# Kernel tuning notes

Hardware: AMD Instinct MI355X
Metric: run time of the kernel (lower is better)

## Reference

```python
import jax, jax.numpy as jnp
import numpy as np

SMOOTH = 1e-06
LAMBDA_FOCAL = 1.0
LAMBDA_DICE = 1.0
LAMBDA_BOUNDARY = 0.5
LAMBDA_CONTRASTIVE = 0.1
ALPHA = 0.25
GAMMA = 2.0
NUM_IDS = 32  # instance ids in [0, NUM_IDS); 0 = background


def _sobel_grad(x):
    """Kornia-style normalized sobel spatial gradient with replicate padding.
    x: [B,1,H,W] -> (gx, gy) each [B,1,H,W]."""
    kx = jnp.array([[-1., 0., 1.], [-2., 0., 2.], [-1., 0., 1.]], x.dtype) / 8.0  # abs-sum normalized
    ky = kx.T
    k = jnp.stack([kx, ky])[:, None]  # [2,1,3,3]
    xp = jnp.pad(x, ((0, 0), (0, 0), (1, 1), (1, 1)), mode='edge')
    out = jax.lax.conv_general_dilated(xp, k, (1, 1), 'VALID',
                                       dimension_numbers=('NCHW', 'OIHW', 'NCHW'))
    return out[:, 0:1], out[:, 1:2]


def _forward(predictions, targets, instance_masks):
    p = jnp.clip(jax.nn.sigmoid(predictions), SMOOTH, 1.0 - SMOOTH)  # [B,H,W]
    t = jnp.clip(targets, 0.0, 1.0)

    # ---- focal loss ----
    bce = -(t * jnp.log(p) + (1.0 - t) * jnp.log1p(-p))
    pt = jnp.where(t == 1.0, p, 1.0 - p)
    focal_w = (1.0 - pt) ** GAMMA
    alpha_w = jnp.where(t == 1.0, ALPHA, 1.0 - ALPHA)
    focal = jnp.mean(alpha_w * focal_w * bce)

    # ---- dice loss ----
    inter = jnp.sum(p * t)
    dice = 1.0 - (2.0 * inter + SMOOTH) / (jnp.sum(p) + jnp.sum(t) + SMOOTH)

    # ---- boundary loss (sobel gradient magnitude + direction) ----
    p4, t4 = p[:, None], t[:, None]  # [B,1,H,W]
    tgx, tgy = _sobel_grad(t4)
    pgx, pgy = _sobel_grad(p4)
    tmag = jnp.sqrt(tgx ** 2 + tgy ** 2 + 1e-6)
    pmag = jnp.sqrt(pgx ** 2 + pgy ** 2 + 1e-6)
    bw = 1.0 + 5.0 * tmag
    loss_mag = jnp.mean((pmag * bw - tmag * bw) ** 2)
    mask = (tmag > 0.1).astype(p.dtype)
    cos = (tgx / tmag) * (pgx / pmag) + (tgy / tmag) * (pgy / pmag)
    msum = jnp.sum(mask)
    dir_loss = jnp.where(msum > 0, jnp.sum((1.0 - cos) * mask) / jnp.maximum(msum, 1.0), 0.0)
    boundary = loss_mag + dir_loss

    # ---- instance contrastive loss (segment-mean + pairwise exp distance) ----
    B = p.shape[0]
    ids = instance_masks.reshape(B, -1).astype(jnp.int32)
    flat_ids = (ids + jnp.arange(B, dtype=jnp.int32)[:, None] * NUM_IDS).reshape(-1)
    pf = p.reshape(-1)
    sums = jax.ops.segment_sum(pf, flat_ids, num_segments=B * NUM_IDS).reshape(B, NUM_IDS)
    cnts = jax.ops.segment_sum(jnp.ones_like(pf), flat_ids, num_segments=B * NUM_IDS).reshape(B, NUM_IDS)
    means = sums / jnp.maximum(cnts, 1.0)  # [B,K]
    ks = jnp.arange(NUM_IDS)
    valid = (cnts > 0) & (ks[None, :] > 0)  # exclude background id 0
    diff = jnp.abs(means[:, :, None] - means[:, None, :])  # [B,K,K]
    pair = (valid[:, :, None] & valid[:, None, :] & (ks[:, None] < ks[None, :])).astype(p.dtype)
    npairs = jnp.sum(pair, axis=(1, 2))
    csum = jnp.sum(jnp.exp(-diff) * pair, axis=(1, 2))
    contrastive = jnp.sum(jnp.where(npairs > 0, csum / jnp.maximum(npairs, 1.0), 0.0)) / B

    return (LAMBDA_FOCAL * focal + LAMBDA_DICE * dice
            + LAMBDA_BOUNDARY * boundary + LAMBDA_CONTRASTIVE * contrastive)


def setup_inputs() -> dict:
    key = jax.random.key(0)
    k1, k2, k3 = jax.random.split(key, 3)
    B, H, W = 16, 1024, 1024
    predictions = jax.random.normal(k1, (B, H, W), dtype=jnp.float32)
    targets = jnp.round(jax.random.uniform(k2, (B, H, W), dtype=jnp.float32))  # binary masks
    instance_masks = jax.random.randint(k3, (B, H, W), 0, NUM_IDS, dtype=jnp.int32)
    return {"predictions": predictions, "targets": targets, "instance_masks": instance_masks}


def reference(predictions, targets, instance_masks):
    return _forward(predictions, targets, instance_masks)
```

## Files before the change

kernel.cpp:

```cpp
#include <hip/hip_runtime.h>
#include <math.h>

#define HH 1024
#define WW 1024
#define BB 16
#define RR 8
#define NID 32
#define NPX (1ull * BB * HH * WW)
#define CBIT 41
#define SSCALE 262144.0f
#define INV_SSCALE 3.814697265625e-06f


__device__ __forceinline__ float fast_rcp(float x) {
  float r; asm("v_rcp_f32 %0, %1" : "=v"(r) : "v"(x)); return r;
}
__device__ __forceinline__ float fast_rsq(float x) {
  float r; asm("v_rsq_f32 %0, %1" : "=v"(r) : "v"(x)); return r;
}
__device__ __forceinline__ float sigc(float x) {
  return fast_rcp(1.f + __expf(-x));
}

__global__ __launch_bounds__(256, 3) void seg_main(
    const float* __restrict__ pred, const float* __restrict__ targ,
    const int* __restrict__ ids, float* __restrict__ acc,
    unsigned long long* __restrict__ seg_pack) {
  __shared__ unsigned long long s_pack[NID];
  __shared__ float red[4][8];
  __shared__ float2 ttab[256];

  const int tid = threadIdx.x;
  const int b  = blockIdx.x >> 7;
  const int rg = blockIdx.x & 127;
  const int h0 = rg * RR;
  const int w0 = tid * 4;
  const int wl = (w0 == 0) ? 0 : w0 - 1;
  const int wr = (w0 == WW - 4) ? WW - 1 : w0 + 4;

  if (tid < NID) s_pack[tid] = 0ull;
  {
    float tgx = fmaf((float)(tid & 15), 0.125f, -0.5f);
    float tgy = fmaf((float)(tid >> 4), 0.125f, -0.5f);
    float m2t = tgx * tgx + tgy * tgy + 1e-6f;
    float rst = fast_rsq(m2t);
    ttab[tid] = make_float2(m2t * rst, rst);
  }
  __syncthreads();

  const size_t base = (size_t)b * HH * WW;
  const float*  pb  = pred + base;
  const float*  tb  = targ + base;
  const int4*   ib4 = (const int4*)(ids + base);

  float facc = 0.f, iacc = 0.f, pacc = 0.f, macc = 0.f, dacc = 0.f;
  int   tcnt = 0, kcnt = 0;

  float Pa0, Pa1, Pa2, Pa3, Pa4, Pa5, Ha1, Ha2, Ha3, Ha4;
  float Pb0, Pb1, Pb2, Pb3, Pb4, Pb5, Hb1, Hb2, Hb3, Hb4;
  float Pc0, Pc1, Pc2, Pc3, Pc4, Pc5, Hc1, Hc2, Hc3, Hc4;
  unsigned int Na, Nb, Nc, HDa, HDb, HDc;
  float4 nx, nt;
  float nxl, nxr, ntl, ntr;
  int4 IDa, IDb;

#define LOADRAW(h)                                                     \
  do { int hh = (h); hh = hh < 0 ? 0 : (hh > HH - 1 ? HH - 1 : hh);    \
    const float* pr  = pb + hh * WW;                                   \
    const float* trw = tb + hh * WW;                                   \
    nx  = *(const float4*)(pr + w0);                                   \
    nxl = pr[wl];  nxr = pr[wr];                                       \
    nt  = *(const float4*)(trw + w0);                                  \
    ntl = trw[wl]; ntr = trw[wr];                                      \
  } while (0)

#define SIG(P, H, N, HD)                                               \
  do {                                                                 \
    P##0 = sigc(nxl);  P##1 = sigc(nx.x); P##2 = sigc(nx.y);           \
    P##3 = sigc(nx.z); P##4 = sigc(nx.w); P##5 = sigc(nxr);            \
    H##1 = P##2 - P##0; H##2 = P##3 - P##1;                            \
    H##3 = P##4 - P##2; H##4 = P##5 - P##3;                            \
    N = (ntl  >= 0.5f ? 0x1u      : 0u)                                \
      | (nt.x >= 0.5f ? 0x10u     : 0u)                                \
      | (nt.y >= 0.5f ? 0x100u    : 0u)                                \
      | (nt.z >= 0.5f ? 0x1000u   : 0u)                                \
      | (nt.w >= 0.5f ? 0x10000u  : 0u)                                \
      | (ntr  >= 0.5f ? 0x100000u : 0u);                               \
    HD = ((N >> 4) + 0x011110u) - (N << 4);                            \
  } while (0)

#define PIX(PB, HA, HB, HC, NB_, GX, GY, c0, c1, c2, idj)              \
  do {                                                                 \
    float p = PB##c1;                                                  \
    const int one = (int)((NB_ >> (4 * (c1))) & 1u);                   \
    float pt = one ? p : 1.f - p;                                      \
    float om = 1.f - pt;                                               \
    facc += (one ? 0.25f : 0.75f) * om * om * (-__logf(pt));           \
    iacc += one ? p : 0.f;                                             \
    pacc += p;                                                         \
    unsigned int gxb = (GX >> (4 * (c1))) & 15u;                       \
    unsigned int gyb = (GY >> (4 * (c1))) & 15u;                       \
    unsigned int tix = gxb | (gyb << 4);                               \
    float2 tt = ttab[tix];               \
    float tmag = tt.x, rst = tt.y;                                     \
    float pgx = (HA##c1 + HC##c1 + 2.f * HB##c1) * 0.125f;             \
    float pgy = (vd##c0 + vd##c2 + 2.f * vd##c1) * 0.125f;             \
    float m2p = pgx * pgx + pgy * pgy + 1e-6f;                         \
    float rsp = fast_rsq(m2p);                                         \
    float pmag = m2p * rsp;                                            \
    float bwv = fmaf(tmag, 5.f, 1.f);                                  \
    float d = (pmag - tmag) * bwv;                                     \
    macc += d * d;                                                     \
    if (tix != 0x44u) {                                                \
      float tgx = fmaf((float)gxb, 0.125f, -0.5f);                     \
      float tgy = fmaf((float)gyb, 0.125f, -0.5f);                     \
      dacc += 1.f - (tgx * pgx + tgy * pgy) * (rst * rsp);             \
      kcnt += 1;                                                       \
    }                                                                  \
    unsigned int q = __float2uint_rn(p * SSCALE);                      \
    atomicAdd(&s_pack[idj], (1ull << CBIT) | (unsigned long long)q);   \
  } while (0)

#define BODY(PA, PB, PC, HA, HB, HC, NA_, NB_, NC_, HDA_, HDB_, HDC_,  \
             IDU, IDN, r)                                              \
  do {                                                                 \
    SIG(PC, HC, NC_, HDC_);                                            \
    if ((r) < RR - 1) {                                                \
      LOADRAW(h0 + (r) + 2);                                           \
      IDN = ib4[(h0 + (r) + 1) * (WW / 4) + tid];                      \
    }                                                                  \
    unsigned int GX = HDA_ + (HDB_ << 1) + HDC_;           \
    unsigned int VD = (NC_ + 0x111111u) - NA_;             \
    unsigned int GY = (VD << 4) + (VD << 1) + (VD >> 4);   \
    tcnt += __popc(NB_ & 0x011110u);                                   \
    float vd0 = PC##0 - PA##0, vd1 = PC##1 - PA##1;                    \
    float vd2 = PC##2 - PA##2, vd3 = PC##3 - PA##3;                    \
    float vd4 = PC##4 - PA##4, vd5 = PC##5 - PA##5;                    \
    PIX(PB, HA, HB, HC, NB_, GX, GY, 0, 1, 2, IDU.x);                  \
    PIX(PB, HA, HB, HC, NB_, GX, GY, 1, 2, 3, IDU.y);                  \
    PIX(PB, HA, HB, HC, NB_, GX, GY, 2, 3, 4, IDU.z);                  \
    PIX(PB, HA, HB, HC, NB_, GX, GY, 3, 4, 5, IDU.w);                  \
    __builtin_amdgcn_sched_barrier(0);                                 \
  } while (0)

  LOADRAW(h0 - 1); SIG(Pa, Ha, Na, HDa);
  LOADRAW(h0);     SIG(Pb, Hb, Nb, HDb);
  LOADRAW(h0 + 1);
  IDa = ib4[h0 * (WW / 4) + tid];
  __builtin_amdgcn_sched_barrier(0);

  BODY(Pa, Pb, Pc, Ha, Hb, Hc, Na, Nb, Nc, HDa, HDb, HDc, IDa, IDb, 0);
  BODY(Pb, Pc, Pa, Hb, Hc, Ha, Nb, Nc, Na, HDb, HDc, HDa, IDb, IDa, 1);
  BODY(Pc, Pa, Pb, Hc, Ha, Hb, Nc, Na, Nb, HDc, HDa, HDb, IDa, IDb, 2);
  BODY(Pa, Pb, Pc, Ha, Hb, Hc, Na, Nb, Nc, HDa, HDb, HDc, IDb, IDa, 3);
  BODY(Pb, Pc, Pa, Hb, Hc, Ha, Nb, Nc, Na, HDb, HDc, HDa, IDa, IDb, 4);
  BODY(Pc, Pa, Pb, Hc, Ha, Hb, Nc, Na, Nb, HDc, HDa, HDb, IDb, IDa, 5);
  BODY(Pa, Pb, Pc, Ha, Hb, Hc, Na, Nb, Nc, HDa, HDb, HDc, IDa, IDb, 6);
  BODY(Pb, Pc, Pa, Hb, Hc, Ha, Nb, Nc, Na, HDb, HDc, HDa, IDb, IDa, 7);

#undef LOADRAW
#undef SIG
#undef PIX
#undef BODY

  float tacc = (float)tcnt;
  float kacc = (float)kcnt;
#define WRED(x)                                                        \
  do { _Pragma("unroll")                                               \
    for (int off = 32; off > 0; off >>= 1) x += __shfl_down(x, off, 64); \
  } while (0)
  WRED(facc); WRED(iacc); WRED(pacc); WRED(tacc);
  WRED(macc); WRED(dacc); WRED(kacc);
#undef WRED
  int wave = tid >> 6, lane = tid & 63;
  if (lane == 0) {
    red[wave][0] = facc; red[wave][1] = iacc; red[wave][2] = pacc;
    red[wave][3] = tacc; red[wave][4] = macc; red[wave][5] = dacc;
    red[wave][6] = kacc;
  }
  __syncthreads();
  if (tid < 7) {
    atomicAdd(&acc[tid], red[0][tid] + red[1][tid] + red[2][tid] + red[3][tid]);
  }
  if (tid < NID) {
    atomicAdd(&seg_pack[b * NID + tid], s_pack[tid]);
  }
}

__global__ void seg_final(const float* __restrict__ acc,
                          const unsigned long long* __restrict__ seg_pack,
                          float* __restrict__ out) {
  __shared__ float contr[BB];
  int tid = threadIdx.x;
  int b   = tid >> 4;
  int l16 = tid & 15;
  if (b < BB) {
    float means[NID];
    bool  val[NID];
    #pragma unroll
    for (int k = 0; k < NID; ++k) {
      unsigned long long v = seg_pack[b * NID + k];
      float cnt = (float)(v >> CBIT);
      float sum = (float)(v & ((1ull << CBIT) - 1)) * INV_SSCALE;
      means[k] = sum / fmaxf(cnt, 1.f);
      val[k] = (cnt > 0.f) && (k > 0);
    }
    float csum = 0.f, np = 0.f;
    int cnt = 0;
    #pragma unroll
    for (int k = 0; k < NID; ++k) {
      #pragma unroll
      for (int l = k + 1; l < NID; ++l) {
        if ((cnt & 15) == l16) {
          if (val[k] && val[l]) {
            csum += __expf(-fabsf(means[k] - means[l]));
            np += 1.f;
          }
        }
        ++cnt;
      }
    }
    #pragma unroll
    for (int off = 1; off < 16; off <<= 1) {
      csum += __shfl_xor(csum, off, 16);
      np   += __shfl_xor(np,   off, 16);
    }
    if (l16 == 0) contr[b] = (np > 0.f) ? csum / fmaxf(np, 1.f) : 0.f;
  }
  __syncthreads();
  if (tid == 0) {
    float c = 0.f;
    for (int b2 = 0; b2 < BB; ++b2) c += contr[b2];
    c /= (float)BB;
    float N = (float)NPX;
    float focal = acc[0] / N;
    float dice  = 1.f - (2.f * acc[1] + 1e-6f) / (acc[2] + acc[3] + 1e-6f);
    float dir   = (acc[6] > 0.f) ? acc[5] / fmaxf(acc[6], 1.f) : 0.f;
    float boundary = acc[4] / N + dir;
    out[0] = focal + dice + 0.5f * boundary + 0.1f * c;
  }
}

extern "C" void kernel_launch(void* const* d_in, const int* in_sizes, int n_in,
                              void* d_out, int out_size, void* d_ws, size_t ws_size,
                              hipStream_t stream) {
  const float* pred = (const float*)d_in[0];
  const float* targ = (const float*)d_in[1];
  const int*   ids  = (const int*)d_in[2];
  float* acc = (float*)d_ws;
  unsigned long long* seg_pack = (unsigned long long*)((char*)d_ws + 64);

  hipMemsetAsync(d_ws, 0, 64 + BB * NID * sizeof(unsigned long long), stream);

  int blocks = BB * (HH / RR);
  seg_main<<<blocks, 256, 0, stream>>>(pred, targ, ids, acc, seg_pack);
  seg_final<<<1, 256, 0, stream>>>(acc, seg_pack, (float*)d_out);
}
```

Before: 68.49 us.

## Process eight pixels per thread with 128-thread blocks and byte-packed ids

Each thread now covers eight consecutive columns instead of four, so blocks shrink to 128 threads. The halo loads and sigmoid evaluations on the left and right edges are shared across more pixels, and instance ids are packed into a 64-bit register of bytes. The aim is to cut redundant halo work and per-thread overhead. In exchange, register pressure rises, launch bounds drop to minimum one block, and each block has fewer waves, which may reduce occupancy and latency hiding.

```diff
diff --git a/kernel.cpp b/kernel.cpp
--- a/kernel.cpp
+++ b/kernel.cpp
@@ -11,6 +11,7 @@
 #define SSCALE 262144.0f
 #define INV_SSCALE 3.814697265625e-06f
 
+typedef unsigned long long u64;
 
 __device__ __forceinline__ float fast_rcp(float x) {
   float r; asm("v_rcp_f32 %0, %1" : "=v"(r) : "v"(x)); return r;
@@ -22,29 +23,33 @@
   return fast_rcp(1.f + __expf(-x));
 }
 
-__global__ __launch_bounds__(256, 3) void seg_main(
+__global__ __launch_bounds__(128, 1) void seg_main(
     const float* __restrict__ pred, const float* __restrict__ targ,
     const int* __restrict__ ids, float* __restrict__ acc,
     unsigned long long* __restrict__ seg_pack) {
   __shared__ unsigned long long s_pack[NID];
-  __shared__ float red[4][8];
+  __shared__ float red[2][8];
   __shared__ float2 ttab[256];
 
   const int tid = threadIdx.x;
   const int b  = blockIdx.x >> 7;
   const int rg = blockIdx.x & 127;
   const int h0 = rg * RR;
-  const int w0 = tid * 4;
+  const int w0 = tid * 8;
   const int wl = (w0 == 0) ? 0 : w0 - 1;
-  const int wr = (w0 == WW - 4) ? WW - 1 : w0 + 4;
+  const int wr = (w0 == WW - 8) ? WW - 1 : w0 + 8;
 
   if (tid < NID) s_pack[tid] = 0ull;
   {
-    float tgx = fmaf((float)(tid & 15), 0.125f, -0.5f);
-    float tgy = fmaf((float)(tid >> 4), 0.125f, -0.5f);
-    float m2t = tgx * tgx + tgy * tgy + 1e-6f;
-    float rst = fast_rsq(m2t);
-    ttab[tid] = make_float2(m2t * rst, rst);
+    #pragma unroll
+    for (int q = 0; q < 2; ++q) {
+      int e = tid + q * 128;
+      float tgx = fmaf((float)(e & 15), 0.125f, -0.5f);
+      float tgy = fmaf((float)(e >> 4), 0.125f, -0.5f);
+      float m2t = tgx * tgx + tgy * tgy + 1e-6f;
+      float rst = fast_rsq(m2t);
+      ttab[e] = make_float2(m2t * rst, rst);
+    }
   }
   __syncthreads();
 
@@ -56,55 +61,84 @@
   float facc = 0.f, iacc = 0.f, pacc = 0.f, macc = 0.f, dacc = 0.f;
   int   tcnt = 0, kcnt = 0;
 
-  float Pa0, Pa1, Pa2, Pa3, Pa4, Pa5, Ha1, Ha2, Ha3, Ha4;
-  float Pb0, Pb1, Pb2, Pb3, Pb4, Pb5, Hb1, Hb2, Hb3, Hb4;
-  float Pc0, Pc1, Pc2, Pc3, Pc4, Pc5, Hc1, Hc2, Hc3, Hc4;
-  unsigned int Na, Nb, Nc, HDa, HDb, HDc;
-  float4 nx, nt;
+  float Pa0, Pa1, Pa2, Pa3, Pa4, Pa5, Pa6, Pa7, Pa8, Pa9;
+  float Pb0, Pb1, Pb2, Pb3, Pb4, Pb5, Pb6, Pb7, Pb8, Pb9;
+  float Pc0, Pc1, Pc2, Pc3, Pc4, Pc5, Pc6, Pc7, Pc8, Pc9;
+  float Ha1, Ha2, Ha3, Ha4, Ha5, Ha6, Ha7, Ha8;
+  float Hb1, Hb2, Hb3, Hb4, Hb5, Hb6, Hb7, Hb8;
+  float Hc1, Hc2, Hc3, Hc4, Hc5, Hc6, Hc7, Hc8;
+  unsigned int NLa, NLb, NLc, NHa, NHb, NHc;
+  unsigned int DLa, DLb, DLc, DHa, DHb, DHc;
+  float4 nx0, nx1, nt0, nt1;
   float nxl, nxr, ntl, ntr;
-  int4 IDa, IDb;
+  u64 IDa, IDb;
 
 #define LOADRAW(h)                                                     \
   do { int hh = (h); hh = hh < 0 ? 0 : (hh > HH - 1 ? HH - 1 : hh);    \
     const float* pr  = pb + hh * WW;                                   \
     const float* trw = tb + hh * WW;                                   \
-    nx  = *(const float4*)(pr + w0);                                   \
+    nx0 = *(const float4*)(pr + w0);                                   \
+    nx1 = *(const float4*)(pr + w0 + 4);                               \
     nxl = pr[wl];  nxr = pr[wr];                                       \
-    nt  = *(const float4*)(trw + w0);                                  \
+    nt0 = *(const float4*)(trw + w0);                                  \
+    nt1 = *(const float4*)(trw + w0 + 4);                              \
     ntl = trw[wl]; ntr = trw[wr];                                      \
   } while (0)
 
-#define SIG(P, H, N, HD)                                               \
+#define LOADID(h, D)                                                   \
   do {                                                                 \
-    P##0 = sigc(nxl);  P##1 = sigc(nx.x); P##2 = sigc(nx.y);           \
-    P##3 = sigc(nx.z); P##4 = sigc(nx.w); P##5 = sigc(nxr);            \
-    H##1 = P##2 - P##0; H##2 = P##3 - P##1;                            \
-    H##3 = P##4 - P##2; H##4 = P##5 - P##3;                            \
-    N = (ntl  >= 0.5f ? 0x1u      : 0u)                                \
-      | (nt.x >= 0.5f ? 0x10u     : 0u)                                \
-      | (nt.y >= 0.5f ? 0x100u    : 0u)                                \
-      | (nt.z >= 0.5f ? 0x1000u   : 0u)                                \
-      | (nt.w >= 0.5f ? 0x10000u  : 0u)                                \
-      | (ntr  >= 0.5f ? 0x100000u : 0u);                               \
-    HD = ((N >> 4) + 0x011110u) - (N << 4);                            \
-  } while (0)
-
-#define PIX(PB, HA, HB, HC, NB_, GX, GY, c0, c1, c2, idj)              \
+    int4 qa = ib4[(h) * (WW / 4) + 2 * tid];                           \
+    int4 qb = ib4[(h) * (WW / 4) + 2 * tid + 1];                       \
+    unsigned int lo = (unsigned)qa.x | ((unsigned)qa.y << 8)           \
+                    | ((unsigned)qa.z << 16) | ((unsigned)qa.w << 24); \
+    unsigned int hi = (unsigned)qb.x | ((unsigned)qb.y << 8)           \
+                    | ((unsigned)qb.z << 16) | ((unsigned)qb.w << 24); \
+    D = (u64)lo | ((u64)hi << 32);                                     \
+  } while (0)
+
+#define SIG(C)                                                         \
   do {                                                                 \
-    float p = PB##c1;                                                  \
-    const int one = (int)((NB_ >> (4 * (c1))) & 1u);                   \
+    P##C##0 = sigc(nxl);   P##C##1 = sigc(nx0.x);                      \
+    P##C##2 = sigc(nx0.y); P##C##3 = sigc(nx0.z);                      \
+    P##C##4 = sigc(nx0.w); P##C##5 = sigc(nx1.x);                      \
+    P##C##6 = sigc(nx1.y); P##C##7 = sigc(nx1.z);                      \
+    P##C##8 = sigc(nx1.w); P##C##9 = sigc(nxr);                        \
+    H##C##1 = P##C##2 - P##C##0; H##C##2 = P##C##3 - P##C##1;          \
+    H##C##3 = P##C##4 - P##C##2; H##C##4 = P##C##5 - P##C##3;          \
+    H##C##5 = P##C##6 - P##C##4; H##C##6 = P##C##7 - P##C##5;          \
+    H##C##7 = P##C##8 - P##C##6; H##C##8 = P##C##9 - P##C##7;          \
+    NL##C = (ntl   >= 0.5f ? 0x1u      : 0u)                           \
+          | (nt0.x >= 0.5f ? 0x10u     : 0u)                           \
+          | (nt0.y >= 0.5f ? 0x100u    : 0u)                           \
+          | (nt0.z >= 0.5f ? 0x1000u   : 0u)                           \
+          | (nt0.w >= 0.5f ? 0x10000u  : 0u)                           \
+          | (nt1.x >= 0.5f ? 0x100000u : 0u);                          \
+    NH##C = (nt0.w >= 0.5f ? 0x1u      : 0u)                           \
+          | (nt1.x >= 0.5f ? 0x10u     : 0u)                           \
+          | (nt1.y >= 0.5f ? 0x100u    : 0u)                           \
+          | (nt1.z >= 0.5f ? 0x1000u   : 0u)                           \
+          | (nt1.w >= 0.5f ? 0x10000u  : 0u)                           \
+          | (ntr   >= 0.5f ? 0x100000u : 0u);                          \
+    DL##C = ((NL##C >> 4) + 0x011110u) - (NL##C << 4);                 \
+    DH##C = ((NH##C >> 4) + 0x011110u) - (NH##C << 4);                 \
+  } while (0)
+
+#define PIX(A, B, C, N_, GX_, GY_, nib, wa, wb, wc, k, IDU)            \
+  do {                                                                 \
+    float p = P##B##wb;                                                \
+    const int one = (int)((N_ >> (4 * (nib))) & 1u);                   \
     float pt = one ? p : 1.f - p;                                      \
     float om = 1.f - pt;                                               \
     facc += (one ? 0.25f : 0.75f) * om * om * (-__logf(pt));           \
     iacc += one ? p : 0.f;                                             \
     pacc += p;                                                         \
-    unsigned int gxb = (GX >> (4 * (c1))) & 15u;                       \
-    unsigned int gyb = (GY >> (4 * (c1))) & 15u;                       \
+    unsigned int gxb = (GX_ >> (4 * (nib))) & 15u;                     \
+    unsigned int gyb = (GY_ >> (4 * (nib))) & 15u;                     \
     unsigned int tix = gxb | (gyb << 4);                               \
     float2 tt = ttab[tix];               \
     float tmag = tt.x, rst = tt.y;                                     \
-    float pgx = (HA##c1 + HC##c1 + 2.f * HB##c1) * 0.125f;             \
-    float pgy = (vd##c0 + vd##c2 + 2.f * vd##c1) * 0.125f;             \
+    float pgx = (H##A##wb + H##C##wb + 2.f * H##B##wb) * 0.125f;       \
+    float pgy = (vd##wa + vd##wc + 2.f * vd##wb) * 0.125f;             \
     float m2p = pgx * pgx + pgy * pgy + 1e-6f;                         \
     float rsp = fast_rsq(m2p);                                         \
     float pmag = m2p * rsp;                                            \
@@ -117,48 +151,58 @@
       dacc += 1.f - (tgx * pgx + tgy * pgy) * (rst * rsp);             \
       kcnt += 1;                                                       \
     }                                                                  \
+    unsigned int idj = (unsigned int)(IDU >> (8 * (k))) & 31u;         \
     unsigned int q = __float2uint_rn(p * SSCALE);                      \
     atomicAdd(&s_pack[idj], (1ull << CBIT) | (unsigned long long)q);   \
   } while (0)
 
-#define BODY(PA, PB, PC, HA, HB, HC, NA_, NB_, NC_, HDA_, HDB_, HDC_,  \
-             IDU, IDN, r)                                              \
+#define BODY(A, B, C, IDU, IDN, r)                                     \
   do {                                                                 \
-    SIG(PC, HC, NC_, HDC_);                                            \
+    SIG(C);                                                            \
     if ((r) < RR - 1) {                                                \
       LOADRAW(h0 + (r) + 2);                                           \
-      IDN = ib4[(h0 + (r) + 1) * (WW / 4) + tid];                      \
+      LOADID(h0 + (r) + 1, IDN);                                       \
     }                                                                  \
-    unsigned int GX = HDA_ + (HDB_ << 1) + HDC_;           \
-    unsigned int VD = (NC_ + 0x111111u) - NA_;             \
-    unsigned int GY = (VD << 4) + (VD << 1) + (VD >> 4);   \
-    tcnt += __popc(NB_ & 0x011110u);                                   \
-    float vd0 = PC##0 - PA##0, vd1 = PC##1 - PA##1;                    \
-    float vd2 = PC##2 - PA##2, vd3 = PC##3 - PA##3;                    \
-    float vd4 = PC##4 - PA##4, vd5 = PC##5 - PA##5;                    \
-    PIX(PB, HA, HB, HC, NB_, GX, GY, 0, 1, 2, IDU.x);                  \
-    PIX(PB, HA, HB, HC, NB_, GX, GY, 1, 2, 3, IDU.y);                  \
-    PIX(PB, HA, HB, HC, NB_, GX, GY, 2, 3, 4, IDU.z);                  \
-    PIX(PB, HA, HB, HC, NB_, GX, GY, 3, 4, 5, IDU.w);                  \
+    unsigned int GXl = DL##A + (DL##B << 1) + DL##C;                   \
+    unsigned int VDl = (NL##C + 0x111111u) - NL##A;                    \
+    unsigned int GYl = (VDl << 4) + (VDl << 1) + (VDl >> 4);           \
+    unsigned int GXh = DH##A + (DH##B << 1) + DH##C;                   \
+    unsigned int VDh = (NH##C + 0x111111u) - NH##A;                    \
+    unsigned int GYh = (VDh << 4) + (VDh << 1) + (VDh >> 4);           \
+    tcnt += __popc(NL##B & 0x011110u) + __popc(NH##B & 0x011110u);     \
+    float vd0 = P##C##0 - P##A##0, vd1 = P##C##1 - P##A##1;            \
+    float vd2 = P##C##2 - P##A##2, vd3 = P##C##3 - P##A##3;            \
+    float vd4 = P##C##4 - P##A##4, vd5 = P##C##5 - P##A##5;            \
+    float vd6 = P##C##6 - P##A##6, vd7 = P##C##7 - P##A##7;            \
+    float vd8 = P##C##8 - P##A##8, vd9 = P##C##9 - P##A##9;            \
+    PIX(A, B, C, NL##B, GXl, GYl, 1, 0, 1, 2, 0, IDU);                 \
+    PIX(A, B, C, NL##B, GXl, GYl, 2, 1, 2, 3, 1, IDU);                 \
+    PIX(A, B, C, NL##B, GXl, GYl, 3, 2, 3, 4, 2, IDU);                 \
+    PIX(A, B, C, NL##B, GXl, GYl, 4, 3, 4, 5, 3, IDU);                 \
+    PIX(A, B, C, NH##B, GXh, GYh, 1, 4, 5, 6, 4, IDU);                 \
+    PIX(A, B, C, NH##B, GXh, GYh, 2, 5, 6, 7, 5, IDU);                 \
+    PIX(A, B, C, NH##B, GXh, GYh, 3, 6, 7, 8, 6, IDU);                 \
+    PIX(A, B, C, NH##B, GXh, GYh, 4, 7, 8, 9, 7, IDU);                 \
     __builtin_amdgcn_sched_barrier(0);                                 \
   } while (0)
 
-  LOADRAW(h0 - 1); SIG(Pa, Ha, Na, HDa);
-  LOADRAW(h0);     SIG(Pb, Hb, Nb, HDb);
+  LOADRAW(h0 - 1); SIG(a);
+  LOADRAW(h0);     SIG(b);
   LOADRAW(h0 + 1);
-  IDa = ib4[h0 * (WW / 4) + tid];
+  LOADID(h0, IDa);
   __builtin_amdgcn_sched_barrier(0);
 
-  BODY(Pa, Pb, Pc, Ha, Hb, Hc, Na, Nb, Nc, HDa, HDb, HDc, IDa, IDb, 0);
-  BODY(Pb, Pc, Pa, Hb, Hc, Ha, Nb, Nc, Na, HDb, HDc, HDa, IDb, IDa, 1);
-  BODY(Pc, Pa, Pb, Hc, Ha, Hb, Nc, Na, Nb, HDc, HDa, HDb, IDa, IDb, 2);
-  BODY(Pa, Pb, Pc, Ha, Hb, Hc, Na, Nb, Nc, HDa, HDb, HDc, IDb, IDa, 3);
-  BODY(Pb, Pc, Pa, Hb, Hc, Ha, Nb, Nc, Na, HDb, HDc, HDa, IDa, IDb, 4);
-  BODY(Pc, Pa, Pb, Hc, Ha, Hb, Nc, Na, Nb, HDc, HDa, HDb, IDb, IDa, 5);
-  BODY(Pa, Pb, Pc, Ha, Hb, Hc, Na, Nb, Nc, HDa, HDb, HDc, IDa, IDb, 6);
-  BODY(Pb, Pc, Pa, Hb, Hc, Ha, Nb, Nc, Na, HDb, HDc, HDa, IDb, IDa, 7);
+  BODY(a, b, c, IDa, IDb, 0);
+  BODY(b, c, a, IDb, IDa, 1);
+  BODY(c, a, b, IDa, IDb, 2);
+  BODY(a, b, c, IDb, IDa, 3);
+  BODY(b, c, a, IDa, IDb, 4);
+  BODY(c, a, b, IDb, IDa, 5);
+  BODY(a, b, c, IDa, IDb, 6);
+  BODY(b, c, a, IDb, IDa, 7);
 
 #undef LOADRAW
+#undef LOADID
 #undef SIG
 #undef PIX
 #undef BODY
@@ -180,7 +224,7 @@
   }
   __syncthreads();
   if (tid < 7) {
-    atomicAdd(&acc[tid], red[0][tid] + red[1][tid] + red[2][tid] + red[3][tid]);
+    atomicAdd(&acc[tid], red[0][tid] + red[1][tid]);
   }
   if (tid < NID) {
     atomicAdd(&seg_pack[b * NID + tid], s_pack[tid]);
@@ -253,6 +297,6 @@
   hipMemsetAsync(d_ws, 0, 64 + BB * NID * sizeof(unsigned long long), stream);
 
   int blocks = BB * (HH / RR);
-  seg_main<<<blocks, 256, 0, stream>>>(pred, targ, ids, acc, seg_pack);
+  seg_main<<<blocks, 128, 0, stream>>>(pred, targ, ids, acc, seg_pack);
   seg_final<<<1, 256, 0, stream>>>(acc, seg_pack, (float*)d_out);
 }
```

Measured after the change: 93.46 us. 1.36x slower.
